# Optimization experiments

Hardware: AMD Instinct MI355X
Metric: run time of the kernel (lower is better)

The kernel has to match this reference:

```python
import jax, jax.numpy as jnp
import numpy as np

N = 100000        # nodes
E = 1600000       # directed edges (before self loops)
F = 128           # input node features
H1, H2, H3 = 64, 32, 16
G = 64            # graphs in batch
EPS = 1e-5
NEG_SLOPE = 0.2


def setup_inputs():
    key = jax.random.key(0)
    ks = jax.random.split(key, 16)
    def rn(k, shape, scale=1.0):
        return jax.random.normal(k, shape, dtype=jnp.float32) * scale
    inp = {}
    inp['x'] = rn(ks[0], (N, F))
    inp['edge_index'] = jax.random.randint(ks[1], (2, E), 0, N)
    inp['batch'] = jnp.sort(jax.random.randint(ks[2], (N,), 0, G))
    dims = [(F, H1), (H1, H2), (H2, H3)]
    i = 3
    for li, (fi, fo) in enumerate(dims, start=1):
        s = 1.0 / np.sqrt(fi)
        kk = jax.random.split(ks[i], 3)
        inp[f'Wl{li}'] = rn(kk[0], (fi, fo), s)
        inp[f'bl{li}'] = jnp.zeros((fo,), jnp.float32)
        inp[f'Wr{li}'] = rn(kk[1], (fi, fo), s)
        inp[f'br{li}'] = jnp.zeros((fo,), jnp.float32)
        inp[f'att{li}'] = rn(kk[2], (fo,), 1.0 / np.sqrt(fo))
        inp[f'bias{li}'] = jnp.zeros((fo,), jnp.float32)
        inp[f'gamma{li}'] = jnp.ones((fo,), jnp.float32)
        inp[f'beta{li}'] = jnp.zeros((fo,), jnp.float32)
        i += 1
    inp['linW'] = rn(ks[i], (H3, 1), 0.25)
    inp['linb'] = jnp.zeros((1,), jnp.float32)
    return inp


def _gatv2(x, Wl, bl, Wr, br, att, bias, src, dst):
    # PyG GATv2Conv, heads=1: e_ij = a^T LeakyReLU(Wl x_j + Wr x_i)
    xl = x @ Wl + bl                         # [N, H] source transform
    xr = x @ Wr + br                         # [N, H] target transform
    e = jax.nn.leaky_relu(xl[src] + xr[dst], NEG_SLOPE) @ att   # [E']
    # numerically stable segment softmax over incoming edges of dst
    emax = jax.ops.segment_max(e, dst, num_segments=N)
    w = jnp.exp(e - emax[dst])
    denom = jax.ops.segment_sum(w, dst, num_segments=N)
    alpha = w / (denom[dst] + 1e-16)         # [E']
    out = jax.ops.segment_sum(alpha[:, None] * xl[src], dst, num_segments=N)
    return out + bias


def _batchnorm(x, gamma, beta):
    mu = jnp.mean(x, axis=0)
    var = jnp.var(x, axis=0)
    return (x - mu) * jax.lax.rsqrt(var + EPS) * gamma + beta


def reference(x, edge_index, batch,
              Wl1, bl1, Wr1, br1, att1, bias1, gamma1, beta1,
              Wl2, bl2, Wr2, br2, att2, bias2, gamma2, beta2,
              Wl3, bl3, Wr3, br3, att3, bias3, gamma3, beta3,
              linW, linb):
    # add self loops once (PyG GATv2Conv default add_self_loops=True)
    loops = jnp.arange(N, dtype=edge_index.dtype)
    src = jnp.concatenate([edge_index[0], loops])
    dst = jnp.concatenate([edge_index[1], loops])

    h = _gatv2(x, Wl1, bl1, Wr1, br1, att1, bias1, src, dst)
    h = jax.nn.relu(_batchnorm(h, gamma1, beta1))
    h = _gatv2(h, Wl2, bl2, Wr2, br2, att2, bias2, src, dst)
    h = jax.nn.relu(_batchnorm(h, gamma2, beta2))
    h = _gatv2(h, Wl3, bl3, Wr3, br3, att3, bias3, src, dst)
    h = jax.nn.relu(_batchnorm(h, gamma3, beta3))

    # global mean pool over graphs
    sums = jax.ops.segment_sum(h, batch, num_segments=G)          # [G, 16]
    cnts = jax.ops.segment_sum(jnp.ones((N,), h.dtype), batch, num_segments=G)
    pooled = sums / jnp.maximum(cnts, 1.0)[:, None]
    return pooled @ linW + linb                                   # [G, 1]
```

## Files before the change

kernel.cpp:

```cpp
#include <hip/hip_runtime.h>
#include <hip/hip_bf16.h>


static constexpr int G_ = 64;

typedef short bfrag __attribute__((ext_vector_type(8)));
typedef float facc  __attribute__((ext_vector_type(4)));

__device__ __forceinline__ float asfloat_(unsigned int u) {
  union { unsigned int i; float f; } c; c.i = u; return c.f;
}
__device__ __forceinline__ unsigned short f2bf(float f) {
  union { float f; unsigned int i; } c;
  c.f = f;
  unsigned int r = c.i + 0x7FFFu + ((c.i >> 16) & 1u);
  return (unsigned short)(r >> 16);
}

__device__ __forceinline__ void load_bf4(const unsigned short* p, float* f) {
  uint2 q = *reinterpret_cast<const uint2*>(p);
  f[0] = asfloat_(q.x << 16); f[1] = asfloat_(q.x & 0xFFFF0000u);
  f[2] = asfloat_(q.y << 16); f[3] = asfloat_(q.y & 0xFFFF0000u);
}

__global__ __launch_bounds__(256) void pack_all(
    const float* __restrict__ Wl1, const float* __restrict__ Wr1,
    const float* __restrict__ bl1, const float* __restrict__ br1,
    const float* __restrict__ Wl2, const float* __restrict__ Wr2,
    const float* __restrict__ bl2, const float* __restrict__ br2,
    const float* __restrict__ Wl3, const float* __restrict__ Wr3,
    const float* __restrict__ bl3, const float* __restrict__ br3,
    unsigned short* __restrict__ Wt1, float* __restrict__ bc1,
    unsigned short* __restrict__ Wt2, float* __restrict__ bc2,
    unsigned short* __restrict__ Wt3, float* __restrict__ bc3) {
  int i = blockIdx.x * 256 + threadIdx.x;
  if (i < 128 * 128) { int c = i >> 7, k = i & 127;
    Wt1[i] = f2bf((c < 64) ? Wl1[k * 64 + c] : Wr1[k * 64 + (c - 64)]); }
  if (i < 128) bc1[i] = (i < 64) ? bl1[i] : br1[i - 64];
  if (i < 64 * 64) { int c = i >> 6, k = i & 63;
    Wt2[i] = f2bf((c < 32) ? Wl2[k * 32 + c] : Wr2[k * 32 + (c - 32)]); }
  if (i < 64) bc2[i] = (i < 32) ? bl2[i] : br2[i - 32];
  if (i < 32 * 32) { int c = i >> 5, k = i & 31;
    Wt3[i] = f2bf((c < 16) ? Wl3[k * 16 + c] : Wr3[k * 16 + (c - 16)]); }
  if (i < 32) bc3[i] = (i < 16) ? bl3[i] : br3[i - 16];
}

__global__ __launch_bounds__(256) void edge_hist(
    const int* __restrict__ ei, int* __restrict__ deg, int E, int Etot, int N) {
  int p = blockIdx.x & 7;
  int q = blockIdx.x >> 3;
  int nbq = gridDim.x >> 3;
  float scale = 8.0f / (float)N;
  for (int i = q * 256 + threadIdx.x; i < Etot; i += nbq * 256) {
    int dst = (i < E) ? ei[E + i] : (i - E);
    int pp = min((int)((float)dst * scale), 7);
    if (pp == p) atomicAdd(&deg[dst], 1);
  }
}

__global__ __launch_bounds__(256) void scan1(
    const int* __restrict__ deg, int* __restrict__ part, int* __restrict__ bsums, int n) {
  __shared__ int ts[256];
  int t = threadIdx.x, b = blockIdx.x;
  int base = b * 1024 + t * 4;
  int d[4];
#pragma unroll
  for (int q = 0; q < 4; q++) d[q] = (base + q < n) ? deg[base + q] : 0;
  int s = d[0] + d[1] + d[2] + d[3];
  ts[t] = s;
  __syncthreads();
  for (int o = 1; o < 256; o <<= 1) {
    int v = (t >= o) ? ts[t - o] : 0;
    __syncthreads();
    ts[t] += v;
    __syncthreads();
  }
  int incl = ts[t];
  if (t == 255) bsums[b] = incl;
  int run = incl - s;
#pragma unroll
  for (int q = 0; q < 4; q++) {
    if (base + q < n) part[base + q] = run;
    run += d[q];
  }
}

__global__ void scan2(int* bsums, int nb) {
  __shared__ int s[256];
  int t = threadIdx.x;
  int v = (t < nb) ? bsums[t] : 0;
  s[t] = v;
  __syncthreads();
  for (int o = 1; o < 256; o <<= 1) {
    int u = (t >= o) ? s[t - o] : 0;
    __syncthreads();
    s[t] += u;
    __syncthreads();
  }
  if (t < nb) bsums[t] = s[t] - v;
}

__global__ __launch_bounds__(256) void scan3(
    int* __restrict__ rp, int* __restrict__ cur, const int* __restrict__ bsums,
    int n, int Etot) {
  int i = blockIdx.x * 256 + threadIdx.x;
  if (i < n) {
    int v = rp[i] + bsums[i >> 10];
    rp[i] = v; cur[i] = v;
  }
  if (i == 0) rp[n] = Etot;
}

__global__ __launch_bounds__(256) void scatter_edges(
    const int* __restrict__ ei, int* __restrict__ cur, int* __restrict__ ssrc,
    int E, int Etot, int N) {
  int p = blockIdx.x & 7;
  int q = blockIdx.x >> 3;
  int nbq = gridDim.x >> 3;
  float scale = 8.0f / (float)N;
  for (int i = q * 256 + threadIdx.x; i < Etot; i += nbq * 256) {
    int dst = (i < E) ? ei[E + i] : (i - E);
    int pp = min((int)((float)dst * scale), 7);
    if (pp != p) continue;
    int src = (i < E) ? ei[i] : (i - E);
    int pos = atomicAdd(&cur[dst], 1);
    ssrc[pos] = src;
  }
}

template <int FI, int FO, int AMODE>
__global__ __launch_bounds__(256) void gemm_mfma(
    const void* __restrict__ Ain, const float* __restrict__ ssb,
    const unsigned short* __restrict__ Wt, const float* __restrict__ bcat,
    unsigned short* __restrict__ XL, unsigned short* __restrict__ XR, int N) {
  constexpr int NT = FO / 16;
  constexpr int KS = FI / 32;
  constexpr int H = FO / 2;
  int tid = threadIdx.x;
  int w = tid >> 6;
  int lr = tid & 15;
  int lg = (tid & 63) >> 4;
  int n0 = blockIdx.x * 64;
  int arow = min(n0 + w * 16 + lr, N - 1);

  facc acc[NT];
#pragma unroll
  for (int t = 0; t < NT; t++)
#pragma unroll
    for (int e = 0; e < 4; e++) acc[t][e] = 0.f;

#pragma unroll
  for (int ks = 0; ks < KS; ks++) {
    int k0 = ks * 32 + lg * 8;
    bfrag a;
    if constexpr (AMODE == 0) {
      const unsigned short* Ab = (const unsigned short*)Ain;
      a = *reinterpret_cast<const bfrag*>(&Ab[(size_t)arow * FI + k0]);
    } else {
      const float* Af = (const float*)Ain;
      const float* p = &Af[(size_t)arow * FI + k0];
      float4 lo = *reinterpret_cast<const float4*>(p);
      float4 hi = *reinterpret_cast<const float4*>(p + 4);
      float f[8] = {lo.x, lo.y, lo.z, lo.w, hi.x, hi.y, hi.z, hi.w};
      if constexpr (AMODE == 2) {
        float4 sc0 = *reinterpret_cast<const float4*>(&ssb[k0]);
        float4 sc1 = *reinterpret_cast<const float4*>(&ssb[k0 + 4]);
        float4 sh0 = *reinterpret_cast<const float4*>(&ssb[FI + k0]);
        float4 sh1 = *reinterpret_cast<const float4*>(&ssb[FI + k0 + 4]);
        float sc[8] = {sc0.x, sc0.y, sc0.z, sc0.w, sc1.x, sc1.y, sc1.z, sc1.w};
        float sh[8] = {sh0.x, sh0.y, sh0.z, sh0.w, sh1.x, sh1.y, sh1.z, sh1.w};
#pragma unroll
        for (int e = 0; e < 8; e++) f[e] = fmaxf(fmaf(f[e], sc[e], sh[e]), 0.f);
      }
      union { bfrag v; unsigned short u[8]; } cv;
#pragma unroll
      for (int e = 0; e < 8; e++) cv.u[e] = f2bf(f[e]);
      a = cv.v;
    }
#pragma unroll
    for (int t = 0; t < NT; t++) {
      bfrag b = *reinterpret_cast<const bfrag*>(&Wt[(size_t)(t * 16 + lr) * FI + k0]);
      acc[t] = __builtin_amdgcn_mfma_f32_16x16x32_bf16(a, b, acc[t], 0, 0, 0);
    }
  }

#pragma unroll
  for (int t = 0; t < NT; t++) {
    int col = t * 16 + lr;
    float bias = bcat[col];
    unsigned short* dstbuf = (t < NT / 2) ? XL : XR;
    int cc = (t < NT / 2) ? col : (col - H);
#pragma unroll
    for (int r = 0; r < 4; r++) {
      int n = n0 + w * 16 + lg * 4 + r;
      if (n < N) dstbuf[(size_t)n * H + cc] = f2bf(acc[t][r] + bias);
    }
  }
}

__device__ __forceinline__ float lrelu02(float z) {
  return fmaxf(z, 0.2f * z);
}

template <int H, bool UN2>
__global__ __launch_bounds__(256) void gat_agg4(
    const unsigned short* __restrict__ XL, const unsigned short* __restrict__ XR,
    const float* __restrict__ att, const float* __restrict__ bias,
    const int* __restrict__ rp, const int* __restrict__ ssrc,
    float* __restrict__ out, int N) {
  constexpr int L = H / 4;
  constexpr int C = 64 / L;
  constexpr int STEP = UN2 ? 2 * C : C;
  int v = blockIdx.x * 4 + (threadIdx.x >> 6);
  if (v >= N) return;
  int lane = threadIdx.x & 63;
  int fl = lane % L;
  int sub = lane / L;

  float xr[4];
  load_bf4(&XR[(size_t)v * H + fl * 4], xr);
  const float4 a4 = *reinterpret_cast<const float4*>(&att[fl * 4]);
  int beg = rp[v], end = rp[v + 1];

  float mA = -3.0e38f, dA = 0.f, accA[4] = {0.f, 0.f, 0.f, 0.f};
  float mB = -3.0e38f, dB = 0.f, accB[4] = {0.f, 0.f, 0.f, 0.f};

  auto edge = [&](int j, float& m, float& d, float (&acc)[4]) {
    int u = ssrc[j];
    float xl[4];
    load_bf4(&XL[(size_t)u * H + fl * 4], xl);
    float t = a4.x * lrelu02(xl[0] + xr[0]);
    t = fmaf(a4.y, lrelu02(xl[1] + xr[1]), t);
    t = fmaf(a4.z, lrelu02(xl[2] + xr[2]), t);
    t = fmaf(a4.w, lrelu02(xl[3] + xr[3]), t);
#pragma unroll
    for (int o = L / 2; o >= 1; o >>= 1) t += __shfl_xor(t, o);
    float diff = t - m;
    if (diff > 8.f) {
      float sc = __expf(-diff);
      d *= sc;
#pragma unroll
      for (int e = 0; e < 4; e++) acc[e] *= sc;
      m = t; diff = 0.f;
    }
    float w = __expf(diff);
    d += w;
#pragma unroll
    for (int e = 0; e < 4; e++) acc[e] = fmaf(w, xl[e], acc[e]);
  };

  for (int j = beg + sub; j < end; j += STEP) {
    edge(j, mA, dA, accA);
    if (UN2) {
      int j2 = j + C;
      if (j2 < end) edge(j2, mB, dB, accB);
    }
  }

  if (UN2) {
    float mn = fmaxf(mA, mB);
    float s1 = __expf(mA - mn), s2 = __expf(mB - mn);
    dA = dA * s1 + dB * s2;
#pragma unroll
    for (int e = 0; e < 4; e++) accA[e] = accA[e] * s1 + accB[e] * s2;
    mA = mn;
  }

#pragma unroll
  for (int o = L; o < 64; o <<= 1) {
    float mo = __shfl_xor(mA, o);
    float d2 = __shfl_xor(dA, o);
    float a0 = __shfl_xor(accA[0], o);
    float a1 = __shfl_xor(accA[1], o);
    float a2 = __shfl_xor(accA[2], o);
    float a3 = __shfl_xor(accA[3], o);
    float mn = fmaxf(mA, mo);
    float s1 = __expf(mA - mn), s2 = __expf(mo - mn);
    dA = dA * s1 + d2 * s2;
    accA[0] = accA[0] * s1 + a0 * s2;
    accA[1] = accA[1] * s1 + a1 * s2;
    accA[2] = accA[2] * s1 + a2 * s2;
    accA[3] = accA[3] * s1 + a3 * s2;
    mA = mn;
  }

  if (lane < L) {
    float inv = 1.f / (dA + 1e-16f);
    const float4 b4 = *reinterpret_cast<const float4*>(&bias[fl * 4]);
    float4 o4 = make_float4(fmaf(accA[0], inv, b4.x), fmaf(accA[1], inv, b4.y),
                            fmaf(accA[2], inv, b4.z), fmaf(accA[3], inv, b4.w));
    *reinterpret_cast<float4*>(&out[(size_t)v * H + fl * 4]) = o4;
  }
}

template <int H>
__global__ __launch_bounds__(256) void bn_stats(
    const float* __restrict__ X, float* __restrict__ stats, int N) {
  __shared__ float ls[256], ls2[256];
  int tid = threadIdx.x;
  int h = tid % H;
  constexpr int RPB = 256 / H;
  int r0 = blockIdx.x * RPB + tid / H;
  float s = 0.f, s2 = 0.f;
  for (int n = r0; n < N; n += gridDim.x * RPB) {
    float val = X[(size_t)n * H + h];
    s += val; s2 += val * val;
  }
  ls[tid] = s; ls2[tid] = s2;
  __syncthreads();
  if (tid < H) {
    for (int g = 1; g < RPB; g++) { s += ls[tid + g * H]; s2 += ls2[tid + g * H]; }
    atomicAdd(&stats[h], s);
    atomicAdd(&stats[H + h], s2);
  }
}

__global__ void bn_finalize(
    const float* __restrict__ stats, const float* __restrict__ gamma,
    const float* __restrict__ beta, float* __restrict__ ss, int H, int N) {
  int h = threadIdx.x;
  if (h < H) {
    float mean = stats[h] / (float)N;
    float var = stats[H + h] / (float)N - mean * mean;
    float istd = rsqrtf(var + 1e-5f);
    float sc = gamma[h] * istd;
    ss[h] = sc;
    ss[H + h] = beta[h] - mean * sc;
  }
}

__global__ __launch_bounds__(256) void pool_kernel(
    const float* __restrict__ X, const float* __restrict__ ss,
    const int* __restrict__ batch, float* __restrict__ pool,
    float* __restrict__ cnt, int N) {
  __shared__ float lp[G_ * 16];
  __shared__ float lc[G_];
  int tid = threadIdx.x;
  for (int j = tid; j < G_ * 16; j += 256) lp[j] = 0.f;
  if (tid < G_) lc[tid] = 0.f;
  __syncthreads();
  int tot = N * 16;
  for (int i = blockIdx.x * 256 + tid; i < tot; i += gridDim.x * 256) {
    int n = i >> 4, h = i & 15;
    int g = batch[n];
    float t = X[i] * ss[h] + ss[16 + h];
    t = (t > 0.f) ? t : 0.f;
    atomicAdd(&lp[g * 16 + h], t);
    if (h == 0) atomicAdd(&lc[g], 1.0f);
  }
  __syncthreads();
  for (int j = tid; j < G_ * 16; j += 256) atomicAdd(&pool[j], lp[j]);
  if (tid < G_) atomicAdd(&cnt[tid], lc[tid]);
}

__global__ void final_linear(
    const float* __restrict__ pool, const float* __restrict__ cnt,
    const float* __restrict__ linW, const float* __restrict__ linb,
    float* __restrict__ out) {
  int g = threadIdx.x;
  if (g < G_) {
    float c = fmaxf(cnt[g], 1.0f);
    float acc = 0.f;
    for (int h = 0; h < 16; h++) acc += (pool[g * 16 + h] / c) * linW[h];
    out[g] = acc + linb[0];
  }
}

extern "C" void kernel_launch(void* const* d_in, const int* in_sizes, int n_in,
                              void* d_out, int out_size, void* d_ws, size_t ws_size,
                              hipStream_t stream) {
  const float* x = (const float*)d_in[0];
  const int* ei = (const int*)d_in[1];
  const int* batch = (const int*)d_in[2];
  const int N = in_sizes[0] / 128;
  const int E = in_sizes[1] / 2;
  const int Etot = E + N;

  char* wsb = (char*)d_ws;
  size_t off = 0;
  auto alloc = [&](size_t bytes) -> void* {
    void* p = wsb + off;
    off += (bytes + 255) & ~(size_t)255;
    return p;
  };
  unsigned short* XLb = (unsigned short*)alloc((size_t)64 * N * 2);
  unsigned short* XRb = (unsigned short*)alloc((size_t)64 * N * 2);
  float* R2 = (float*)alloc((size_t)64 * N * 4);
  int* row_ptr = (int*)alloc((size_t)(N + 1) * 4);
  int* cursor = (int*)alloc((size_t)N * 4);
  int* bsums = (int*)alloc(4096);
  int* ssrc = (int*)alloc((size_t)Etot * 4);
  unsigned short* Wt1 = (unsigned short*)alloc(16384 * 2);
  float* bc1 = (float*)alloc(128 * 4);
  unsigned short* Wt2 = (unsigned short*)alloc(4096 * 2);
  float* bc2 = (float*)alloc(64 * 4);
  unsigned short* Wt3 = (unsigned short*)alloc(1024 * 2);
  float* bc3 = (float*)alloc(32 * 4);
  float* ss = (float*)alloc(256 * 4);
  size_t zelems = (size_t)N + 3 * 128 + G_ * 16 + G_;
  char* zb = (char*)alloc(zelems * 4);
  int* deg = (int*)zb;
  float* stats1 = (float*)(zb + (size_t)N * 4);
  float* stats2 = stats1 + 128;
  float* stats3 = stats2 + 128;
  float* pool = stats3 + 128;
  float* cnt = pool + G_ * 16;

  const float* Wl1 = (const float*)d_in[3];  const float* bl1 = (const float*)d_in[4];
  const float* Wr1 = (const float*)d_in[5];  const float* br1 = (const float*)d_in[6];
  const float* att1 = (const float*)d_in[7]; const float* bias1 = (const float*)d_in[8];
  const float* g1 = (const float*)d_in[9];   const float* b1 = (const float*)d_in[10];
  const float* Wl2 = (const float*)d_in[11]; const float* bl2 = (const float*)d_in[12];
  const float* Wr2 = (const float*)d_in[13]; const float* br2 = (const float*)d_in[14];
  const float* att2 = (const float*)d_in[15]; const float* bias2 = (const float*)d_in[16];
  const float* g2 = (const float*)d_in[17];  const float* b2 = (const float*)d_in[18];
  const float* Wl3 = (const float*)d_in[19]; const float* bl3 = (const float*)d_in[20];
  const float* Wr3 = (const float*)d_in[21]; const float* br3 = (const float*)d_in[22];
  const float* att3 = (const float*)d_in[23]; const float* bias3 = (const float*)d_in[24];
  const float* g3 = (const float*)d_in[25];  const float* b3 = (const float*)d_in[26];
  const float* linW = (const float*)d_in[27]; const float* linb = (const float*)d_in[28];
  float* out = (float*)d_out;

  int nb = (N + 1023) / 1024;
  int nnodeblk = (N + 3) / 4;
  int ngemm = (N + 63) / 64;

  pack_all<<<64, 256, 0, stream>>>(Wl1, Wr1, bl1, br1, Wl2, Wr2, bl2, br2,
                                   Wl3, Wr3, bl3, br3, Wt1, bc1, Wt2, bc2, Wt3, bc3);
  hipMemsetAsync(zb, 0, zelems * 4, stream);

  edge_hist<<<4096, 256, 0, stream>>>(ei, deg, E, Etot, N);
  scan1<<<nb, 256, 0, stream>>>(deg, row_ptr, bsums, N);
  scan2<<<1, 256, 0, stream>>>(bsums, nb);
  scan3<<<(N + 255) / 256, 256, 0, stream>>>(row_ptr, cursor, bsums, N, Etot);
  scatter_edges<<<4096, 256, 0, stream>>>(ei, cursor, ssrc, E, Etot, N);

  gemm_mfma<128, 128, 1><<<ngemm, 256, 0, stream>>>(x, nullptr, Wt1, bc1, XLb, XRb, N);
  gat_agg4<64, true><<<nnodeblk, 256, 0, stream>>>(XLb, XRb, att1, bias1, row_ptr, ssrc, R2, N);
  bn_stats<64><<<512, 256, 0, stream>>>(R2, stats1, N);
  bn_finalize<<<1, 64, 0, stream>>>(stats1, g1, b1, ss, 64, N);

  gemm_mfma<64, 64, 2><<<ngemm, 256, 0, stream>>>(R2, ss, Wt2, bc2, XLb, XRb, N);
  gat_agg4<32, true><<<nnodeblk, 256, 0, stream>>>(XLb, XRb, att2, bias2, row_ptr, ssrc, R2, N);
  bn_stats<32><<<512, 256, 0, stream>>>(R2, stats2, N);
  bn_finalize<<<1, 64, 0, stream>>>(stats2, g2, b2, ss, 32, N);

  gemm_mfma<32, 32, 2><<<ngemm, 256, 0, stream>>>(R2, ss, Wt3, bc3, XLb, XRb, N);
  gat_agg4<16, false><<<nnodeblk, 256, 0, stream>>>(XLb, XRb, att3, bias3, row_ptr, ssrc, R2, N);
  bn_stats<16><<<512, 256, 0, stream>>>(R2, stats3, N);
  bn_finalize<<<1, 64, 0, stream>>>(stats3, g3, b3, ss, 16, N);

  pool_kernel<<<2048, 256, 0, stream>>>(R2, ss, batch, pool, cnt, N);
  final_linear<<<1, 64, 0, stream>>>(pool, cnt, linW, linb, out);
}
```

Baseline: 510.1 us.

## Store aggregation outputs as bf16, fuse BN finalize, add chunked softmax aggregator

Several changes at once. The intermediate layer outputs R2 are now stored as bf16 instead of fp32, which halves traffic in the aggregation write, BN stats, next GEMM and pool reads. The BN finalize kernels are removed; scale and shift are computed inside the consuming GEMM (staged in shared memory) and inside the pool kernel. A new gat_agg6 aggregator for layers 2 and 3 batches ITER edges per chunk, applies one max rescale per chunk instead of per edge, and combines lanes with plain sums. The risk is extra rounding error from bf16 intermediates and redundant per-block finalize work.

```diff
diff --git a/kernel.cpp b/kernel.cpp
--- a/kernel.cpp
+++ b/kernel.cpp
@@ -3,6 +3,7 @@
 
 
 static constexpr int G_ = 64;
+static constexpr float EPS_ = 1e-5f;
 
 typedef short bfrag __attribute__((ext_vector_type(8)));
 typedef float facc  __attribute__((ext_vector_type(4)));
@@ -15,6 +16,9 @@
   c.f = f;
   unsigned int r = c.i + 0x7FFFu + ((c.i >> 16) & 1u);
   return (unsigned short)(r >> 16);
+}
+__device__ __forceinline__ unsigned int pack2bf(float a, float b) {
+  return (unsigned int)f2bf(a) | ((unsigned int)f2bf(b) << 16);
 }
 
 __device__ __forceinline__ void load_bf4(const unsigned short* p, float* f) {
@@ -130,13 +134,26 @@
 
 template <int FI, int FO, int AMODE>
 __global__ __launch_bounds__(256) void gemm_mfma(
-    const void* __restrict__ Ain, const float* __restrict__ ssb,
+    const void* __restrict__ Ain, const float* __restrict__ stats,
+    const float* __restrict__ gamma, const float* __restrict__ beta,
     const unsigned short* __restrict__ Wt, const float* __restrict__ bcat,
     unsigned short* __restrict__ XL, unsigned short* __restrict__ XR, int N) {
   constexpr int NT = FO / 16;
   constexpr int KS = FI / 32;
   constexpr int H = FO / 2;
+  __shared__ float ssh[2 * FI];
   int tid = threadIdx.x;
+  if constexpr (AMODE == 2) {
+    if (tid < FI) {
+      float inv = 1.0f / (float)N;
+      float mean = stats[tid] * inv;
+      float var = stats[FI + tid] * inv - mean * mean;
+      float sc = gamma[tid] * rsqrtf(var + EPS_);
+      ssh[tid] = sc;
+      ssh[FI + tid] = beta[tid] - mean * sc;
+    }
+    __syncthreads();
+  }
   int w = tid >> 6;
   int lr = tid & 15;
   int lg = (tid & 63) >> 4;
@@ -153,28 +170,32 @@
   for (int ks = 0; ks < KS; ks++) {
     int k0 = ks * 32 + lg * 8;
     bfrag a;
-    if constexpr (AMODE == 0) {
-      const unsigned short* Ab = (const unsigned short*)Ain;
-      a = *reinterpret_cast<const bfrag*>(&Ab[(size_t)arow * FI + k0]);
-    } else {
+    if constexpr (AMODE == 1) {
       const float* Af = (const float*)Ain;
       const float* p = &Af[(size_t)arow * FI + k0];
       float4 lo = *reinterpret_cast<const float4*>(p);
       float4 hi = *reinterpret_cast<const float4*>(p + 4);
-      float f[8] = {lo.x, lo.y, lo.z, lo.w, hi.x, hi.y, hi.z, hi.w};
-      if constexpr (AMODE == 2) {
-        float4 sc0 = *reinterpret_cast<const float4*>(&ssb[k0]);
-        float4 sc1 = *reinterpret_cast<const float4*>(&ssb[k0 + 4]);
-        float4 sh0 = *reinterpret_cast<const float4*>(&ssb[FI + k0]);
-        float4 sh1 = *reinterpret_cast<const float4*>(&ssb[FI + k0 + 4]);
-        float sc[8] = {sc0.x, sc0.y, sc0.z, sc0.w, sc1.x, sc1.y, sc1.z, sc1.w};
-        float sh[8] = {sh0.x, sh0.y, sh0.z, sh0.w, sh1.x, sh1.y, sh1.z, sh1.w};
-#pragma unroll
-        for (int e = 0; e < 8; e++) f[e] = fmaxf(fmaf(f[e], sc[e], sh[e]), 0.f);
-      }
       union { bfrag v; unsigned short u[8]; } cv;
-#pragma unroll
-      for (int e = 0; e < 8; e++) cv.u[e] = f2bf(f[e]);
+      cv.u[0] = f2bf(lo.x); cv.u[1] = f2bf(lo.y);
+      cv.u[2] = f2bf(lo.z); cv.u[3] = f2bf(lo.w);
+      cv.u[4] = f2bf(hi.x); cv.u[5] = f2bf(hi.y);
+      cv.u[6] = f2bf(hi.z); cv.u[7] = f2bf(hi.w);
+      a = cv.v;
+    } else {
+      const unsigned short* Ab = (const unsigned short*)Ain;
+      float f[8];
+      load_bf4(&Ab[(size_t)arow * FI + k0], f);
+      load_bf4(&Ab[(size_t)arow * FI + k0 + 4], f + 4);
+      float4 sc0 = *reinterpret_cast<const float4*>(&ssh[k0]);
+      float4 sc1 = *reinterpret_cast<const float4*>(&ssh[k0 + 4]);
+      float4 sh0 = *reinterpret_cast<const float4*>(&ssh[FI + k0]);
+      float4 sh1 = *reinterpret_cast<const float4*>(&ssh[FI + k0 + 4]);
+      float sc[8] = {sc0.x, sc0.y, sc0.z, sc0.w, sc1.x, sc1.y, sc1.z, sc1.w};
+      float sh[8] = {sh0.x, sh0.y, sh0.z, sh0.w, sh1.x, sh1.y, sh1.z, sh1.w};
+      union { bfrag v; unsigned short u[8]; } cv;
+#pragma unroll
+      for (int e = 0; e < 8; e++)
+        cv.u[e] = f2bf(fmaxf(fmaf(f[e], sc[e], sh[e]), 0.f));
       a = cv.v;
     }
 #pragma unroll
@@ -202,15 +223,15 @@
   return fmaxf(z, 0.2f * z);
 }
 
-template <int H, bool UN2>
+template <int H>
 __global__ __launch_bounds__(256) void gat_agg4(
     const unsigned short* __restrict__ XL, const unsigned short* __restrict__ XR,
     const float* __restrict__ att, const float* __restrict__ bias,
     const int* __restrict__ rp, const int* __restrict__ ssrc,
-    float* __restrict__ out, int N) {
+    unsigned short* __restrict__ out, int N) {
   constexpr int L = H / 4;
   constexpr int C = 64 / L;
-  constexpr int STEP = UN2 ? 2 * C : C;
+  constexpr int STEP = 2 * C;
   int v = blockIdx.x * 4 + (threadIdx.x >> 6);
   if (v >= N) return;
   int lane = threadIdx.x & 63;
@@ -251,13 +272,11 @@
 
   for (int j = beg + sub; j < end; j += STEP) {
     edge(j, mA, dA, accA);
-    if (UN2) {
-      int j2 = j + C;
-      if (j2 < end) edge(j2, mB, dB, accB);
-    }
-  }
-
-  if (UN2) {
+    int j2 = j + C;
+    if (j2 < end) edge(j2, mB, dB, accB);
+  }
+
+  {
     float mn = fmaxf(mA, mB);
     float s1 = __expf(mA - mn), s2 = __expf(mB - mn);
     dA = dA * s1 + dB * s2;
@@ -287,50 +306,123 @@
   if (lane < L) {
     float inv = 1.f / (dA + 1e-16f);
     const float4 b4 = *reinterpret_cast<const float4*>(&bias[fl * 4]);
-    float4 o4 = make_float4(fmaf(accA[0], inv, b4.x), fmaf(accA[1], inv, b4.y),
-                            fmaf(accA[2], inv, b4.z), fmaf(accA[3], inv, b4.w));
-    *reinterpret_cast<float4*>(&out[(size_t)v * H + fl * 4]) = o4;
+    uint2 o;
+    o.x = pack2bf(fmaf(accA[0], inv, b4.x), fmaf(accA[1], inv, b4.y));
+    o.y = pack2bf(fmaf(accA[2], inv, b4.z), fmaf(accA[3], inv, b4.w));
+    *reinterpret_cast<uint2*>(&out[(size_t)v * H + fl * 4]) = o;
+  }
+}
+
+template <int H, int ITER>
+__global__ __launch_bounds__(256) void gat_agg6(
+    const unsigned short* __restrict__ XL, const unsigned short* __restrict__ XR,
+    const float* __restrict__ att, const float* __restrict__ bias,
+    const int* __restrict__ rp, const int* __restrict__ ssrc,
+    unsigned short* __restrict__ out, int N) {
+  constexpr int L = H / 4;
+  constexpr int C = 64 / L;
+  constexpr int CHUNK = C * ITER;
+  int v = blockIdx.x * 4 + (threadIdx.x >> 6);
+  if (v >= N) return;
+  int lane = threadIdx.x & 63;
+  int fl = lane % L;
+  int sub = lane / L;
+
+  float xr[4];
+  load_bf4(&XR[(size_t)v * H + fl * 4], xr);
+  const float4 a4 = *reinterpret_cast<const float4*>(&att[fl * 4]);
+  int beg = rp[v], end = rp[v + 1];
+
+  float m = -3.0e38f, d = 0.f, acc[4] = {0.f, 0.f, 0.f, 0.f};
+
+  for (int cb = beg; cb < end; cb += CHUNK) {
+    float xb[ITER][4];
+    float tl[ITER];
+    float mc = -3.0e38f;
+#pragma unroll
+    for (int it = 0; it < ITER; it++) {
+      int j = cb + it * C + sub;
+      bool valid = (j < end);
+      int jj = valid ? j : (end - 1);
+      int u = ssrc[jj];
+      load_bf4(&XL[(size_t)u * H + fl * 4], xb[it]);
+      float t = a4.x * lrelu02(xb[it][0] + xr[0]);
+      t = fmaf(a4.y, lrelu02(xb[it][1] + xr[1]), t);
+      t = fmaf(a4.z, lrelu02(xb[it][2] + xr[2]), t);
+      t = fmaf(a4.w, lrelu02(xb[it][3] + xr[3]), t);
+#pragma unroll
+      for (int o = L / 2; o >= 1; o >>= 1) t += __shfl_xor(t, o);
+      tl[it] = valid ? t : -3.0e38f;
+      mc = fmaxf(mc, tl[it]);
+    }
+#pragma unroll
+    for (int o = L; o < 64; o <<= 1) mc = fmaxf(mc, __shfl_xor(mc, o));
+
+    float mn = fmaxf(m, mc);
+    float sc = __expf(m - mn);
+    d *= sc;
+#pragma unroll
+    for (int e = 0; e < 4; e++) acc[e] *= sc;
+    m = mn;
+
+#pragma unroll
+    for (int it = 0; it < ITER; it++) {
+      float w = __expf(tl[it] - m);
+      d += w;
+#pragma unroll
+      for (int e = 0; e < 4; e++) acc[e] = fmaf(w, xb[it][e], acc[e]);
+    }
+  }
+
+#pragma unroll
+  for (int o = L; o < 64; o <<= 1) {
+    d += __shfl_xor(d, o);
+#pragma unroll
+    for (int e = 0; e < 4; e++) acc[e] += __shfl_xor(acc[e], o);
+  }
+
+  if (lane < L) {
+    float inv = 1.f / (d + 1e-16f);
+    const float4 b4 = *reinterpret_cast<const float4*>(&bias[fl * 4]);
+    uint2 o;
+    o.x = pack2bf(fmaf(acc[0], inv, b4.x), fmaf(acc[1], inv, b4.y));
+    o.y = pack2bf(fmaf(acc[2], inv, b4.z), fmaf(acc[3], inv, b4.w));
+    *reinterpret_cast<uint2*>(&out[(size_t)v * H + fl * 4]) = o;
   }
 }
 
 template <int H>
-__global__ __launch_bounds__(256) void bn_stats(
-    const float* __restrict__ X, float* __restrict__ stats, int N) {
-  __shared__ float ls[256], ls2[256];
+__global__ __launch_bounds__(256) void bn_stats_b(
+    const unsigned short* __restrict__ X, float* __restrict__ stats, int N) {
+  constexpr int P = H / 2;
+  constexpr int RPB = 256 / P;
+  __shared__ float lsa[256], lsb[256], lqa[256], lqb[256];
   int tid = threadIdx.x;
-  int h = tid % H;
-  constexpr int RPB = 256 / H;
-  int r0 = blockIdx.x * RPB + tid / H;
-  float s = 0.f, s2 = 0.f;
+  int p = tid % P;
+  int r0 = blockIdx.x * RPB + tid / P;
+  float sa = 0.f, sb = 0.f, qa = 0.f, qb = 0.f;
   for (int n = r0; n < N; n += gridDim.x * RPB) {
-    float val = X[(size_t)n * H + h];
-    s += val; s2 += val * val;
-  }
-  ls[tid] = s; ls2[tid] = s2;
+    unsigned int u = *reinterpret_cast<const unsigned int*>(&X[(size_t)n * H + p * 2]);
+    float a = asfloat_(u << 16), b = asfloat_(u & 0xFFFF0000u);
+    sa += a; qa += a * a; sb += b; qb += b * b;
+  }
+  lsa[tid] = sa; lsb[tid] = sb; lqa[tid] = qa; lqb[tid] = qb;
   __syncthreads();
-  if (tid < H) {
-    for (int g = 1; g < RPB; g++) { s += ls[tid + g * H]; s2 += ls2[tid + g * H]; }
-    atomicAdd(&stats[h], s);
-    atomicAdd(&stats[H + h], s2);
-  }
-}
-
-__global__ void bn_finalize(
-    const float* __restrict__ stats, const float* __restrict__ gamma,
-    const float* __restrict__ beta, float* __restrict__ ss, int H, int N) {
-  int h = threadIdx.x;
-  if (h < H) {
-    float mean = stats[h] / (float)N;
-    float var = stats[H + h] / (float)N - mean * mean;
-    float istd = rsqrtf(var + 1e-5f);
-    float sc = gamma[h] * istd;
-    ss[h] = sc;
-    ss[H + h] = beta[h] - mean * sc;
+  if (tid < P) {
+    for (int g = 1; g < RPB; g++) {
+      sa += lsa[tid + g * P]; sb += lsb[tid + g * P];
+      qa += lqa[tid + g * P]; qb += lqb[tid + g * P];
+    }
+    atomicAdd(&stats[2 * tid], sa);
+    atomicAdd(&stats[2 * tid + 1], sb);
+    atomicAdd(&stats[H + 2 * tid], qa);
+    atomicAdd(&stats[H + 2 * tid + 1], qb);
   }
 }
 
 __global__ __launch_bounds__(256) void pool_kernel(
-    const float* __restrict__ X, const float* __restrict__ ss,
+    const unsigned short* __restrict__ X, const float* __restrict__ stats,
+    const float* __restrict__ gamma, const float* __restrict__ beta,
     const int* __restrict__ batch, float* __restrict__ pool,
     float* __restrict__ cnt, int N) {
   __shared__ float lp[G_ * 16];
@@ -339,14 +431,25 @@
   for (int j = tid; j < G_ * 16; j += 256) lp[j] = 0.f;
   if (tid < G_) lc[tid] = 0.f;
   __syncthreads();
-  int tot = N * 16;
+  int pp = (blockIdx.x * 256 + tid) & 7;
+  float invN = 1.0f / (float)N;
+  float m0 = stats[2 * pp] * invN, m1 = stats[2 * pp + 1] * invN;
+  float v0 = stats[16 + 2 * pp] * invN - m0 * m0;
+  float v1 = stats[16 + 2 * pp + 1] * invN - m1 * m1;
+  float sc0 = gamma[2 * pp] * rsqrtf(v0 + EPS_);
+  float sc1 = gamma[2 * pp + 1] * rsqrtf(v1 + EPS_);
+  float sh0 = beta[2 * pp] - m0 * sc0;
+  float sh1 = beta[2 * pp + 1] - m1 * sc1;
+  int tot = N * 8;
   for (int i = blockIdx.x * 256 + tid; i < tot; i += gridDim.x * 256) {
-    int n = i >> 4, h = i & 15;
+    int n = i >> 3;
     int g = batch[n];
-    float t = X[i] * ss[h] + ss[16 + h];
-    t = (t > 0.f) ? t : 0.f;
-    atomicAdd(&lp[g * 16 + h], t);
-    if (h == 0) atomicAdd(&lc[g], 1.0f);
+    unsigned int u = *reinterpret_cast<const unsigned int*>(&X[(size_t)n * 16 + pp * 2]);
+    float a = fmaxf(fmaf(asfloat_(u << 16), sc0, sh0), 0.f);
+    float b = fmaxf(fmaf(asfloat_(u & 0xFFFF0000u), sc1, sh1), 0.f);
+    atomicAdd(&lp[g * 16 + 2 * pp], a);
+    atomicAdd(&lp[g * 16 + 2 * pp + 1], b);
+    if (pp == 0) atomicAdd(&lc[g], 1.0f);
   }
   __syncthreads();
   for (int j = tid; j < G_ * 16; j += 256) atomicAdd(&pool[j], lp[j]);
@@ -385,7 +488,7 @@
   };
   unsigned short* XLb = (unsigned short*)alloc((size_t)64 * N * 2);
   unsigned short* XRb = (unsigned short*)alloc((size_t)64 * N * 2);
-  float* R2 = (float*)alloc((size_t)64 * N * 4);
+  unsigned short* R2b = (unsigned short*)alloc((size_t)64 * N * 2);
   int* row_ptr = (int*)alloc((size_t)(N + 1) * 4);
   int* cursor = (int*)alloc((size_t)N * 4);
   int* bsums = (int*)alloc(4096);
@@ -396,7 +499,6 @@
   float* bc2 = (float*)alloc(64 * 4);
   unsigned short* Wt3 = (unsigned short*)alloc(1024 * 2);
   float* bc3 = (float*)alloc(32 * 4);
-  float* ss = (float*)alloc(256 * 4);
   size_t zelems = (size_t)N + 3 * 128 + G_ * 16 + G_;
   char* zb = (char*)alloc(zelems * 4);
   int* deg = (int*)zb;
@@ -435,21 +537,21 @@
   scan3<<<(N + 255) / 256, 256, 0, stream>>>(row_ptr, cursor, bsums, N, Etot);
   scatter_edges<<<4096, 256, 0, stream>>>(ei, cursor, ssrc, E, Etot, N);
 
-  gemm_mfma<128, 128, 1><<<ngemm, 256, 0, stream>>>(x, nullptr, Wt1, bc1, XLb, XRb, N);
-  gat_agg4<64, true><<<nnodeblk, 256, 0, stream>>>(XLb, XRb, att1, bias1, row_ptr, ssrc, R2, N);
-  bn_stats<64><<<512, 256, 0, stream>>>(R2, stats1, N);
-  bn_finalize<<<1, 64, 0, stream>>>(stats1, g1, b1, ss, 64, N);
-
-  gemm_mfma<64, 64, 2><<<ngemm, 256, 0, stream>>>(R2, ss, Wt2, bc2, XLb, XRb, N);
-  gat_agg4<32, true><<<nnodeblk, 256, 0, stream>>>(XLb, XRb, att2, bias2, row_ptr, ssrc, R2, N);
-  bn_stats<32><<<512, 256, 0, stream>>>(R2, stats2, N);
-  bn_finalize<<<1, 64, 0, stream>>>(stats2, g2, b2, ss, 32, N);
-
-  gemm_mfma<32, 32, 2><<<ngemm, 256, 0, stream>>>(R2, ss, Wt3, bc3, XLb, XRb, N);
-  gat_agg4<16, false><<<nnodeblk, 256, 0, stream>>>(XLb, XRb, att3, bias3, row_ptr, ssrc, R2, N);
-  bn_stats<16><<<512, 256, 0, stream>>>(R2, stats3, N);
-  bn_finalize<<<1, 64, 0, stream>>>(stats3, g3, b3, ss, 16, N);
-
-  pool_kernel<<<2048, 256, 0, stream>>>(R2, ss, batch, pool, cnt, N);
+  gemm_mfma<128, 128, 1><<<ngemm, 256, 0, stream>>>(
+      x, nullptr, nullptr, nullptr, Wt1, bc1, XLb, XRb, N);
+  gat_agg4<64><<<nnodeblk, 256, 0, stream>>>(XLb, XRb, att1, bias1, row_ptr, ssrc, R2b, N);
+  bn_stats_b<64><<<512, 256, 0, stream>>>(R2b, stats1, N);
+
+  gemm_mfma<64, 64, 2><<<ngemm, 256, 0, stream>>>(
+      R2b, stats1, g1, b1, Wt2, bc2, XLb, XRb, N);
+  gat_agg6<32, 4><<<nnodeblk, 256, 0, stream>>>(XLb, XRb, att2, bias2, row_ptr, ssrc, R2b, N);
+  bn_stats_b<32><<<512, 256, 0, stream>>>(R2b, stats2, N);
+
+  gemm_mfma<32, 32, 2><<<ngemm, 256, 0, stream>>>(
+      R2b, stats2, g2, b2, Wt3, bc3, XLb, XRb, N);
+  gat_agg6<16, 2><<<nnodeblk, 256, 0, stream>>>(XLb, XRb, att3, bias3, row_ptr, ssrc, R2b, N);
+  bn_stats_b<16><<<512, 256, 0, stream>>>(R2b, stats3, N);
+
+  pool_kernel<<<2048, 256, 0, stream>>>(R2b, stats3, g3, b3, batch, pool, cnt, N);
   final_linear<<<1, 64, 0, stream>>>(pool, cnt, linW, linb, out);
 }
```

New measurement: 512.6 us. No clear change (+0.5%).
